# Kernel tuning notes

Hardware: AMD Instinct MI355X
Metric: run time of the kernel (lower is better)

Reference implementation:

```python
import jax, jax.numpy as jnp
import numpy as np

N_NODES = 200000
AVG_DEG = 64
N_EDGES = N_NODES * AVG_DEG
ALPHA = 0.1
DT = 0.01
EPS = 1e-9
DIFF = 10.0
HARD_LO = -jnp.pi / 2
HARD_HI = jnp.pi / 2


def setup_inputs() -> dict:
    key = jax.random.key(0)
    ks = jax.random.split(key, 8)
    xy = jax.random.normal(ks[0], (N_NODES, 2), dtype=jnp.float32)
    xy_dot_old = jax.random.normal(ks[1], (N_NODES, 2), dtype=jnp.float32)
    scale = 2.0 * np.pi
    phase = (jax.random.uniform(ks[2], (N_NODES,), dtype=jnp.float32) * 2 - 1) * scale
    w = (jax.random.uniform(ks[3], (N_NODES,), dtype=jnp.float32) * 2 - 1) * scale
    amplitudes = (jax.random.uniform(ks[4], (N_NODES,), dtype=jnp.float32) * 2 - 1) * scale
    ha = jax.random.normal(ks[5], (N_NODES,), dtype=jnp.float32)
    edge_src = jnp.sort(jax.random.randint(ks[6], (N_EDGES,), 0, N_NODES, dtype=jnp.int32))
    edge_dst = jax.random.randint(ks[7], (N_EDGES,), 0, N_NODES, dtype=jnp.int32)
    return {
        "xy": xy,
        "xy_dot_old": xy_dot_old,
        "phase": phase,
        "w": w,
        "amplitudes": amplitudes,
        "ha": ha,
        "edge_src": edge_src,
        "edge_dst": edge_dst,
    }


def reference(xy, xy_dot_old, phase, w, amplitudes, ha, edge_src, edge_dst):
    n = xy.shape[0]
    x, y = xy[:, 0], xy[:, 1]
    xd_old, yd_old = xy_dot_old[:, 0], xy_dot_old[:, 1]

    # per-node gain matrix K_i = [[a, -b], [b, a]]
    r2 = x * x + y * y
    a = ALPHA * (1.0 - r2 * r2)                         # term_a
    zeta = 1.0 - ha * ((xd_old + EPS) / (jnp.abs(xd_old) + EPS))
    b = w / (zeta + EPS)                                # term_b
    kx = a * x - b * y                                  # (K_i @ xy_i).x
    ky = b * x + a * y                                  # (K_i @ xy_i).y

    # edge coupling: R(phase_i - phase_j) @ xy_j, summed over neighbors j of i
    pd = phase[edge_src] - phase[edge_dst]
    c, s = jnp.cos(pd), jnp.sin(pd)
    xj = x[edge_dst]
    yj = y[edge_dst]
    ex = c * xj - s * yj
    ey = s * xj + c * yj
    sum_x = jax.ops.segment_sum(ex, edge_src, num_segments=n)
    sum_y = jax.ops.segment_sum(ey, edge_src, num_segments=n)

    # integrate with rate clamp
    x_dot = jnp.clip(kx + sum_x, xd_old - DIFF, xd_old + DIFF)
    y_dot = jnp.clip(ky + sum_y, yd_old - DIFF, yd_old + DIFF)
    x_new = x + x_dot * DT
    y_new = y + y_dot * DT

    angles = jnp.clip(amplitudes * y_new, HARD_LO, HARD_HI)
    xy_new = jnp.stack([x_new, y_new], axis=-1)
    xy_dot_old_new = xy  # original sets xy_dot_old[i] = old xy[i]
    return angles, xy_new, xy_dot_old_new
```

## Files before the change

### kernel.cpp

```cpp
#include <hip/hip_runtime.h>
#include <math.h>

#define ALPHA  0.1f
#define DT     0.01f
#define EPSV   1e-9f
#define DIFF   10.0f
#define HARD_P 1.5707963267948966f

__global__ void node_pre(const float2* __restrict__ xy,
                         const float*  __restrict__ phase,
                         const int*    __restrict__ src,
                         float2* __restrict__ g,
                         float2* __restrict__ out_xyold,
                         int*    __restrict__ rowptr,
                         int n, int n_edges) {
    int i = blockIdx.x * blockDim.x + threadIdx.x;

    if (i < n) {
        float2 p = xy[i];
        float ph = phase[i];
        float s, c;
        sincosf(ph, &s, &c);
        float2 gv;
        gv.x = p.x * c + p.y * s;
        gv.y = p.y * c - p.x * s;
        g[i] = gv;
        out_xyold[i] = p;
    }

    int n_chunks = (n_edges + 63) >> 6;
    if (i < n_chunks) {
        int base = i << 6;
        int end  = min(base + 64, n_edges);
        int prev = (base == 0) ? -1 : src[base - 1];
        const int4* s4 = (const int4*)(src + base);
        for (int q = 0; q < (end - base + 3) / 4; ++q) {
            int4 v = s4[q];
            int vals[4] = {v.x, v.y, v.z, v.w};
            #pragma unroll
            for (int k = 0; k < 4; ++k) {
                int e = base + 4*q + k;
                if (e >= end) break;
                int cur = vals[k];
                if (cur != prev) {
                    for (int r = prev + 1; r <= cur; ++r) rowptr[r] = e;
                    prev = cur;
                }
            }
        }
        if (end == n_edges) {
            for (int r = prev + 1; r <= n; ++r) rowptr[r] = n_edges;
        }
    }
}

__global__ __launch_bounds__(256) void edge_sum(
        const int*    __restrict__ rowptr,
        const int*    __restrict__ dst,
        const float2* __restrict__ g,
        float2* __restrict__ Gsum,
        int n) {
    const int lane = threadIdx.x & 63;
    const int wid  = threadIdx.x >> 6;
    const int node = blockIdx.x * (blockDim.x >> 6) + wid;
    if (node >= n) return;

    const int e0 = rowptr[node];
    const int e1 = rowptr[node + 1];

    float ax = 0.f, ay = 0.f;
    for (int e = e0 + lane; e < e1; e += 64) {
        int d = dst[e];
        float2 gd = g[d];
        ax += gd.x; ay += gd.y;
    }
    #pragma unroll
    for (int off = 32; off > 0; off >>= 1) {
        ax += __shfl_xor(ax, off);
        ay += __shfl_xor(ay, off);
    }
    if (lane == 0) {
        float2 v; v.x = ax; v.y = ay;
        Gsum[node] = v;
    }
}

__global__ void node_post(const float2* __restrict__ xy,
                          const float2* __restrict__ xyd,
                          const float*  __restrict__ phase,
                          const float*  __restrict__ w,
                          const float*  __restrict__ amps,
                          const float*  __restrict__ ha,
                          const float2* __restrict__ Gsum,
                          float* __restrict__ out,
                          int n) {
    int i = blockIdx.x * blockDim.x + threadIdx.x;
    if (i >= n) return;
    float2 p   = xy[i];
    float2 pdv = xyd[i];
    float x = p.x, y = p.y;
    float xd = pdv.x, yd = pdv.y;

    float r2 = x*x + y*y;
    float a = ALPHA * (1.0f - r2*r2);
    float h = ha[i];
    float zeta = 1.0f - h * ((xd + EPSV) / (fabsf(xd) + EPSV));
    float b = w[i] / (zeta + EPSV);
    float kx = a*x - b*y;
    float ky = b*x + a*y;

    float2 gv = Gsum[i];
    float s, c;
    sincosf(phase[i], &s, &c);
    float sumx = c*gv.x - s*gv.y;
    float sumy = s*gv.x + c*gv.y;

    float xdot = fminf(fmaxf(kx + sumx, xd - DIFF), xd + DIFF);
    float ydot = fminf(fmaxf(ky + sumy, yd - DIFF), yd + DIFF);
    float xn = x + xdot * DT;
    float yn = y + ydot * DT;

    float ang = fminf(fmaxf(amps[i] * yn, -HARD_P), HARD_P);

    out[i] = ang;
    float2* xy_new = (float2*)(out + n);
    float2 v; v.x = xn; v.y = yn;
    xy_new[i] = v;
}

extern "C" void kernel_launch(void* const* d_in, const int* in_sizes, int n_in,
                              void* d_out, int out_size, void* d_ws, size_t ws_size,
                              hipStream_t stream) {
    const float2* xy    = (const float2*)d_in[0];
    const float2* xyd   = (const float2*)d_in[1];
    const float*  phase = (const float*)d_in[2];
    const float*  w     = (const float*)d_in[3];
    const float*  amps  = (const float*)d_in[4];
    const float*  ha    = (const float*)d_in[5];
    const int*    esrc  = (const int*)d_in[6];
    const int*    edst  = (const int*)d_in[7];

    const int n       = in_sizes[2];
    const int n_edges = in_sizes[6];

    float* out = (float*)d_out;

    float2* g      = (float2*)d_ws;
    float2* Gsum   = (float2*)((char*)d_ws + (size_t)n * sizeof(float2));
    int*    rowptr = (int*)((char*)d_ws + (size_t)2 * n * sizeof(float2));

    const int B = 256;
    int n_chunks = (n_edges + 63) >> 6;
    int pre_items = (n > n_chunks) ? n : n_chunks;
    node_pre<<<(pre_items + B - 1) / B, B, 0, stream>>>(
        xy, phase, esrc, g, (float2*)(out + (size_t)3 * n), rowptr, n, n_edges);

    const int nodes_per_block = B / 64;
    edge_sum<<<(n + nodes_per_block - 1) / nodes_per_block, B, 0, stream>>>(
        rowptr, edst, g, Gsum, n);

    node_post<<<(n + B - 1) / B, B, 0, stream>>>(
        xy, xyd, phase, w, amps, ha, Gsum, out, n);
}
```

Baseline: 243.6 us.

## Replace CSR rowptr build and per-node reduction with edge-parallel segmented scan plus atomics

Drops the rowptr construction and the one-wavefront-per-node reduction. Each edge now gets its own thread. A wavefront-wide segmented inclusive scan keyed on the sorted source index sums contributions, and only segment tails do float atomicAdds into a Gsum that is zeroed in node_pre. The aim is to remove the serial rowptr-building work and the idle lanes of per-node wavefronts, since average degree 64 fills only part of each wave. The cost is a 6-step shuffle scan per edge, atomics at wave boundaries, and summation order that is no longer deterministic.

```diff
diff --git a/kernel.cpp b/kernel.cpp
--- a/kernel.cpp
+++ b/kernel.cpp
@@ -9,79 +9,57 @@
 
 __global__ void node_pre(const float2* __restrict__ xy,
                          const float*  __restrict__ phase,
-                         const int*    __restrict__ src,
                          float2* __restrict__ g,
                          float2* __restrict__ out_xyold,
-                         int*    __restrict__ rowptr,
-                         int n, int n_edges) {
+                         float2* __restrict__ Gsum,
+                         int n) {
     int i = blockIdx.x * blockDim.x + threadIdx.x;
+    if (i >= n) return;
+    float2 p = xy[i];
+    float ph = phase[i];
+    float s, c;
+    sincosf(ph, &s, &c);
+    float2 gv;
+    gv.x = p.x * c + p.y * s;
+    gv.y = p.y * c - p.x * s;
+    g[i] = gv;
+    out_xyold[i] = p;
+    float2 z; z.x = 0.f; z.y = 0.f;
+    Gsum[i] = z;
+}
 
-    if (i < n) {
-        float2 p = xy[i];
-        float ph = phase[i];
-        float s, c;
-        sincosf(ph, &s, &c);
-        float2 gv;
-        gv.x = p.x * c + p.y * s;
-        gv.y = p.y * c - p.x * s;
-        g[i] = gv;
-        out_xyold[i] = p;
+__global__ __launch_bounds__(256) void edge_seg(
+        const int*    __restrict__ src,
+        const int*    __restrict__ dst,
+        const float2* __restrict__ g,
+        float* __restrict__ Gsum,
+        int n_edges) {
+    const int e    = blockIdx.x * blockDim.x + threadIdx.x;
+    const int lane = threadIdx.x & 63;
+    const bool valid = (e < n_edges);
+
+    int s = valid ? __builtin_nontemporal_load(src + e) : -1;
+    int d = valid ? __builtin_nontemporal_load(dst + e) : 0;
+
+    float ax = 0.f, ay = 0.f;
+    if (valid) {
+        float2 gd = g[d];
+        ax = gd.x; ay = gd.y;
     }
 
-    int n_chunks = (n_edges + 63) >> 6;
-    if (i < n_chunks) {
-        int base = i << 6;
-        int end  = min(base + 64, n_edges);
-        int prev = (base == 0) ? -1 : src[base - 1];
-        const int4* s4 = (const int4*)(src + base);
-        for (int q = 0; q < (end - base + 3) / 4; ++q) {
-            int4 v = s4[q];
-            int vals[4] = {v.x, v.y, v.z, v.w};
-            #pragma unroll
-            for (int k = 0; k < 4; ++k) {
-                int e = base + 4*q + k;
-                if (e >= end) break;
-                int cur = vals[k];
-                if (cur != prev) {
-                    for (int r = prev + 1; r <= cur; ++r) rowptr[r] = e;
-                    prev = cur;
-                }
-            }
-        }
-        if (end == n_edges) {
-            for (int r = prev + 1; r <= n; ++r) rowptr[r] = n_edges;
-        }
+    #pragma unroll
+    for (int off = 1; off < 64; off <<= 1) {
+        float px = __shfl_up(ax, off);
+        float py = __shfl_up(ay, off);
+        int   ps = __shfl_up(s,  off);
+        if (lane >= off && ps == s) { ax += px; ay += py; }
     }
-}
 
-__global__ __launch_bounds__(256) void edge_sum(
-        const int*    __restrict__ rowptr,
-        const int*    __restrict__ dst,
-        const float2* __restrict__ g,
-        float2* __restrict__ Gsum,
-        int n) {
-    const int lane = threadIdx.x & 63;
-    const int wid  = threadIdx.x >> 6;
-    const int node = blockIdx.x * (blockDim.x >> 6) + wid;
-    if (node >= n) return;
-
-    const int e0 = rowptr[node];
-    const int e1 = rowptr[node + 1];
-
-    float ax = 0.f, ay = 0.f;
-    for (int e = e0 + lane; e < e1; e += 64) {
-        int d = dst[e];
-        float2 gd = g[d];
-        ax += gd.x; ay += gd.y;
-    }
-    #pragma unroll
-    for (int off = 32; off > 0; off >>= 1) {
-        ax += __shfl_xor(ax, off);
-        ay += __shfl_xor(ay, off);
-    }
-    if (lane == 0) {
-        float2 v; v.x = ax; v.y = ay;
-        Gsum[node] = v;
+    int snext = __shfl_down(s, 1);
+    bool tail = (lane == 63) || (snext != s);
+    if (valid && tail) {
+        atomicAdd(&Gsum[2*s],     ax);
+        atomicAdd(&Gsum[2*s + 1], ay);
     }
 }
 
@@ -145,19 +123,15 @@
 
     float* out = (float*)d_out;
 
-    float2* g      = (float2*)d_ws;
-    float2* Gsum   = (float2*)((char*)d_ws + (size_t)n * sizeof(float2));
-    int*    rowptr = (int*)((char*)d_ws + (size_t)2 * n * sizeof(float2));
+    float2* g    = (float2*)d_ws;
+    float2* Gsum = (float2*)((char*)d_ws + (size_t)n * sizeof(float2));
 
     const int B = 256;
-    int n_chunks = (n_edges + 63) >> 6;
-    int pre_items = (n > n_chunks) ? n : n_chunks;
-    node_pre<<<(pre_items + B - 1) / B, B, 0, stream>>>(
-        xy, phase, esrc, g, (float2*)(out + (size_t)3 * n), rowptr, n, n_edges);
+    node_pre<<<(n + B - 1) / B, B, 0, stream>>>(
+        xy, phase, g, (float2*)(out + (size_t)3 * n), Gsum, n);
 
-    const int nodes_per_block = B / 64;
-    edge_sum<<<(n + nodes_per_block - 1) / nodes_per_block, B, 0, stream>>>(
-        rowptr, edst, g, Gsum, n);
+    edge_seg<<<(n_edges + B - 1) / B, B, 0, stream>>>(
+        esrc, edst, g, (float*)Gsum, n_edges);
 
     node_post<<<(n + B - 1) / B, B, 0, stream>>>(
         xy, xyd, phase, w, amps, ha, Gsum, out, n);
```

After: 204.1 us. 16.2% less time.
